# Kernel optimization log

Hardware: AMD Instinct MI355X
Metric: run time of the kernel (lower is better)

## Reference

```python
import jax, jax.numpy as jnp
import numpy as np

D_MODEL = 512
NHEAD = 8
WINDOW = 128
DFF = 2048
LN_EPS = 1e-5


def _layernorm(x, g, b):
    mu = jnp.mean(x, axis=-1, keepdims=True)
    var = jnp.mean(jnp.square(x - mu), axis=-1, keepdims=True)
    return (x - mu) * jax.lax.rsqrt(var + LN_EPS) * g + b


def setup_inputs() -> dict:
    key = jax.random.key(0)
    ks = jax.random.split(key, 8)
    d, dff = D_MODEL, DFF
    s = 0.02
    return {
        "x": jax.random.normal(ks[0], (1, 4096, d), dtype=jnp.float32),
        # weights stored [in, out] (transposed vs torch nn.Linear.weight)
        "qkv_w": jax.random.normal(ks[1], (d, 3 * d), dtype=jnp.float32) * s,
        "qkv_b": jnp.zeros((3 * d,), jnp.float32),
        "out_w": jax.random.normal(ks[2], (d, d), dtype=jnp.float32) * s,
        "out_b": jnp.zeros((d,), jnp.float32),
        "ln1_g": jnp.ones((d,), jnp.float32),
        "ln1_b": jnp.zeros((d,), jnp.float32),
        "w1": jax.random.normal(ks[3], (d, dff), dtype=jnp.float32) * s,
        "b1": jnp.zeros((dff,), jnp.float32),
        "w2": jax.random.normal(ks[4], (dff, d), dtype=jnp.float32) * s,
        "b2": jnp.zeros((d,), jnp.float32),
        "ln2_g": jnp.ones((d,), jnp.float32),
        "ln2_b": jnp.zeros((d,), jnp.float32),
    }


def reference(x, qkv_w, qkv_b, out_w, out_b, ln1_g, ln1_b, w1, b1, w2, b2, ln2_g, ln2_b):
    B, S, d = x.shape
    H = NHEAD
    hd = d // H
    # qkv projection -> [B,S,3,H,hd] -> q,k,v each [B,H,S,hd]
    qkv = (x @ qkv_w + qkv_b).reshape(B, S, 3, H, hd)
    q = jnp.transpose(qkv[:, :, 0], (0, 2, 1, 3))
    k = jnp.transpose(qkv[:, :, 1], (0, 2, 1, 3))
    v = jnp.transpose(qkv[:, :, 2], (0, 2, 1, 3))
    # NOTE: faithful to source, scale is 1/sqrt(d_model), NOT 1/sqrt(head_dim)
    scores = jnp.einsum('bhqd,bhkd->bhqk', q, k) / jnp.sqrt(jnp.float32(d))
    idx = jnp.arange(S)
    band = jnp.abs(idx[:, None] - idx[None, :]) <= WINDOW  # [S,S] window mask
    scores = jnp.where(band[None, None], scores, -jnp.inf)
    attn = jax.nn.softmax(scores, axis=-1)
    o = jnp.einsum('bhqk,bhkd->bhqd', attn, v)
    o = jnp.transpose(o, (0, 2, 1, 3)).reshape(B, S, d)
    attn_out = o @ out_w + out_b
    x1 = _layernorm(x + attn_out, ln1_g, ln1_b)
    ff = jax.nn.relu(x1 @ w1 + b1) @ w2 + b2  # dropout=0 / eval mode
    return _layernorm(x1 + ff, ln2_g, ln2_b)
```

## Files before the change

kernel.cpp:

```cpp
#include <hip/hip_runtime.h>
#include <math.h>

constexpr int D      = 512;
constexpr int NH     = 8;
constexpr int HD     = 64;
constexpr int WIN    = 128;
constexpr int DFF    = 2048;
constexpr int SEQ    = 4096;
constexpr float LN_EPS = 1e-5f;

typedef float f32x4 __attribute__((ext_vector_type(4)));
typedef __bf16 bf16x8 __attribute__((ext_vector_type(8)));

__device__ __forceinline__ unsigned short f2bf(float f) {
    union { float f; unsigned u; } v; v.f = f;
    unsigned r = v.u + 0x7FFF + ((v.u >> 16) & 1);
    return (unsigned short)(r >> 16);
}
__device__ __forceinline__ float bf2f(unsigned short u) {
    union { unsigned u; float f; } v; v.u = (unsigned)u << 16; return v.f;
}

__device__ __forceinline__ void gload16(const void* g, void* l) {
    __builtin_amdgcn_global_load_lds(
        (const __attribute__((address_space(1))) unsigned int*)g,
        (__attribute__((address_space(3))) unsigned int*)l,
        16, 0, 0);
}

__device__ __forceinline__ int xcd_swizzle() {
    const int orig = blockIdx.x + gridDim.x * (blockIdx.y + gridDim.y * blockIdx.z);
    const int nwg  = gridDim.x * gridDim.y * gridDim.z;
    return (orig & 7) * (nwg >> 3) + (orig >> 3);
}

__global__ __launch_bounds__(256) void prep(
    const float* __restrict__ x, unsigned short* __restrict__ xb,
    const float* __restrict__ qkv_w, const float* __restrict__ out_w,
    const float* __restrict__ w1,    const float* __restrict__ w2,
    unsigned short* __restrict__ qkvw_t, unsigned short* __restrict__ outw_t,
    unsigned short* __restrict__ w1_t,   unsigned short* __restrict__ w2_t)
{
    const int b = blockIdx.x;
    if (b < 1024) {
        int i = b * 2048 + threadIdx.x * 8;
        float4 v0 = *(const float4*)(x + i);
        float4 v1 = *(const float4*)(x + i + 4);
        ushort4 u0 = make_ushort4(f2bf(v0.x), f2bf(v0.y), f2bf(v0.z), f2bf(v0.w));
        ushort4 u1 = make_ushort4(f2bf(v1.x), f2bf(v1.y), f2bf(v1.z), f2bf(v1.w));
        *(ushort4*)(xb + i) = u0;
        *(ushort4*)(xb + i + 4) = u1;
        return;
    }
    __shared__ float t[32][33];
    const int b2 = b - 1024;
    const float* W; unsigned short* Wt; int K, N, nt, kt;
    if (b2 < 768)       { W = qkv_w; Wt = qkvw_t; K = 512;  N = 1536; nt = b2 % 48;          kt = b2 / 48; }
    else if (b2 < 1024) { W = out_w; Wt = outw_t; K = 512;  N = 512;  nt = (b2 - 768) % 16;  kt = (b2 - 768) / 16; }
    else if (b2 < 2048) { W = w1;    Wt = w1_t;   K = 512;  N = 2048; nt = (b2 - 1024) % 64; kt = (b2 - 1024) / 64; }
    else                { W = w2;    Wt = w2_t;   K = 2048; N = 512;  nt = (b2 - 2048) % 16; kt = (b2 - 2048) / 16; }
    const int tx = threadIdx.x & 31, ty = threadIdx.x >> 5;
    const int n0 = nt * 32, k0 = kt * 32;
    #pragma unroll
    for (int r = 0; r < 4; ++r)
        t[ty + r * 8][tx] = W[(size_t)(k0 + ty + r * 8) * N + n0 + tx];
    __syncthreads();
    #pragma unroll
    for (int r = 0; r < 4; ++r)
        Wt[(size_t)(n0 + ty + r * 8) * K + k0 + tx] = f2bf(t[tx][ty + r * 8]);
}

__device__ __forceinline__ void stage64_8w(
    const unsigned short* __restrict__ A, const unsigned short* __restrict__ Bt,
    int K, int m0, int n0, int k0, char* buf, int tid)
{
    const int row = tid >> 2;
    const int kb  = (tid & 3) * 16;
    const char* pa = (const char*)A  + ((size_t)(m0 + row) * K + k0) * 2 + kb;
    const char* pb = (const char*)Bt + ((size_t)(n0 + row) * K + k0) * 2 + kb;
    char* dst = buf + tid * 16;
    gload16(pa,      dst);
    gload16(pa + 64, dst + 8192);
    gload16(pb,      dst + 16384);
    gload16(pb + 64, dst + 24576);
}

__device__ __forceinline__ void gemm_core_db8(
    const unsigned short* __restrict__ A, const unsigned short* __restrict__ Bt,
    int K, int m0, int n0, int kbeg, int kend, char* lds, f32x4 acc[4][2])
{
    const int tid  = threadIdx.x;
    const int lane = tid & 63;
    const int wave = tid >> 6;
    const int wr = wave >> 2, wc = wave & 3;
    const int lr = lane & 15, lk = lane >> 4;
    const int aoff = ((wr * 64 + lr) << 6) + (lk << 4);
    const int boff = 16384 + ((wc * 32 + lr) << 6) + (lk << 4);

    stage64_8w(A, Bt, K, m0, n0, kbeg, lds, tid);
    __syncthreads();

    int cur = 0;
    for (int k0 = kbeg; k0 < kend; k0 += 64) {
        char* bufc = lds + cur * 32768;
        if (k0 + 64 < kend)
            stage64_8w(A, Bt, K, m0, n0, k0 + 64, lds + (cur ^ 1) * 32768, tid);

        bf16x8 af[2][4], bfv[2][2];
        #pragma unroll
        for (int m = 0; m < 4; ++m) {
            af[0][m] = *(const bf16x8*)(bufc +        aoff + m * 1024);
            af[1][m] = *(const bf16x8*)(bufc + 8192 + aoff + m * 1024);
        }
        #pragma unroll
        for (int n = 0; n < 2; ++n) {
            bfv[0][n] = *(const bf16x8*)(bufc +        boff + n * 1024);
            bfv[1][n] = *(const bf16x8*)(bufc + 8192 + boff + n * 1024);
        }
        #pragma unroll
        for (int ks = 0; ks < 2; ++ks)
            #pragma unroll
            for (int m = 0; m < 4; ++m)
                #pragma unroll
                for (int n = 0; n < 2; ++n)
                    acc[m][n] = __builtin_amdgcn_mfma_f32_16x16x32_bf16(
                        af[ks][m], bfv[ks][n], acc[m][n], 0, 0, 0);

        __syncthreads();
        cur ^= 1;
    }
}

template <bool RELU, bool OUT_BF16>
__global__ __launch_bounds__(512) void gemm_mfma(
    const unsigned short* __restrict__ A,
    const unsigned short* __restrict__ Bt,
    const float* __restrict__ bias,
    void* __restrict__ Cv, int M, int N, int K)
{
    __shared__ __align__(16) char lds[65536];
    const int lane = threadIdx.x & 63;
    const int wave = threadIdx.x >> 6;
    const int wr = wave >> 2, wc = wave & 3;
    const int lr = lane & 15, lk = lane >> 4;

    const int wg = xcd_swizzle();
    const int bx = wg % gridDim.x, by = wg / gridDim.x;
    const int m0 = by * 128, n0 = bx * 128;

    f32x4 acc[4][2];
    #pragma unroll
    for (int m = 0; m < 4; ++m)
        #pragma unroll
        for (int n = 0; n < 2; ++n) acc[m][n] = f32x4{0.f, 0.f, 0.f, 0.f};

    gemm_core_db8(A, Bt, K, m0, n0, 0, K, lds, acc);

    const int col0 = n0 + wc * 32 + lr;
    const int row0 = m0 + wr * 64 + lk * 4;
    #pragma unroll
    for (int m = 0; m < 4; ++m)
        #pragma unroll
        for (int n = 0; n < 2; ++n) {
            int col = col0 + n * 16;
            float bv = bias[col];
            #pragma unroll
            for (int j = 0; j < 4; ++j) {
                int row = row0 + m * 16 + j;
                float v = acc[m][n][j] + bv;
                if (RELU) v = fmaxf(v, 0.0f);
                if (OUT_BF16)
                    ((unsigned short*)Cv)[(size_t)row * N + col] = f2bf(v);
                else
                    ((float*)Cv)[(size_t)row * N + col] = v;
            }
        }
}

__global__ __launch_bounds__(512) void gemm_splitk(
    const unsigned short* __restrict__ A,
    const unsigned short* __restrict__ Bt,
    const float* __restrict__ bias,
    unsigned short* __restrict__ P, int M, int N, int K, int Kc)
{
    __shared__ __align__(16) char lds[65536];
    const int lane = threadIdx.x & 63;
    const int wave = threadIdx.x >> 6;
    const int wr = wave >> 2, wc = wave & 3;
    const int lr = lane & 15, lk = lane >> 4;

    const int wg = xcd_swizzle();
    const int bx = wg % gridDim.x;
    const int tmp = wg / gridDim.x;
    const int by = tmp % gridDim.y;
    const int zc = tmp / gridDim.y;
    const int m0 = by * 128, n0 = bx * 128;

    f32x4 acc[4][2];
    #pragma unroll
    for (int m = 0; m < 4; ++m)
        #pragma unroll
        for (int n = 0; n < 2; ++n) acc[m][n] = f32x4{0.f, 0.f, 0.f, 0.f};

    gemm_core_db8(A, Bt, K, m0, n0, zc * Kc, zc * Kc + Kc, lds, acc);

    unsigned short* Cp = P + (size_t)zc * M * N;
    const int col0 = n0 + wc * 32 + lr;
    const int row0 = m0 + wr * 64 + lk * 4;
    #pragma unroll
    for (int m = 0; m < 4; ++m)
        #pragma unroll
        for (int n = 0; n < 2; ++n) {
            int col = col0 + n * 16;
            float bv = (zc == 0) ? bias[col] : 0.0f;
            #pragma unroll
            for (int j = 0; j < 4; ++j) {
                int row = row0 + m * 16 + j;
                Cp[(size_t)row * N + col] = f2bf(acc[m][n][j] + bv);
            }
        }
}

__global__ __launch_bounds__(512) void gemm_qkv(
    const unsigned short* __restrict__ A,
    const unsigned short* __restrict__ Bt,
    const float* __restrict__ bias,
    unsigned short* __restrict__ qb,
    unsigned short* __restrict__ kb,
    unsigned short* __restrict__ vtb)
{
    constexpr int N = 3 * D, K = D;
    __shared__ __align__(16) char lds[65536];
    const int lane = threadIdx.x & 63;
    const int wave = threadIdx.x >> 6;
    const int wr = wave >> 2, wc = wave & 3;
    const int lr = lane & 15, lk = lane >> 4;

    const int wg = xcd_swizzle();
    const int bx = wg % gridDim.x, by = wg / gridDim.x;
    const int m0 = by * 128, n0 = bx * 128;

    f32x4 acc[4][2];
    #pragma unroll
    for (int m = 0; m < 4; ++m)
        #pragma unroll
        for (int n = 0; n < 2; ++n) acc[m][n] = f32x4{0.f, 0.f, 0.f, 0.f};

    gemm_core_db8(A, Bt, K, m0, n0, 0, K, lds, acc);

    const int col0 = n0 + wc * 32 + lr;
    const int row0 = m0 + wr * 64 + lk * 4;
    const int region = n0 >> 9;
    #pragma unroll
    for (int m = 0; m < 4; ++m)
        #pragma unroll
        for (int n = 0; n < 2; ++n) {
            const int col = col0 + n * 16;
            const float bv = bias[col];
            const int rowm = row0 + m * 16;
            if (region == 2) {
                const int cc = col - 1024, hh = cc >> 6, dd = cc & 63;
                ushort4 u = make_ushort4(f2bf(acc[m][n][0] + bv),
                                         f2bf(acc[m][n][1] + bv),
                                         f2bf(acc[m][n][2] + bv),
                                         f2bf(acc[m][n][3] + bv));
                *(ushort4*)&vtb[((size_t)(hh * 64 + dd)) * SEQ + rowm] = u;
            } else {
                const int cc = col - region * 512, hh = cc >> 6, dd = cc & 63;
                unsigned short* dst = (region == 0) ? qb : kb;
                #pragma unroll
                for (int j = 0; j < 4; ++j)
                    dst[((size_t)hh * SEQ + rowm + j) * 64 + dd] =
                        f2bf(acc[m][n][j] + bv);
            }
        }
}

__global__ __launch_bounds__(256) void attn_mfma(
    const unsigned short* __restrict__ qb,
    const unsigned short* __restrict__ kb,
    const unsigned short* __restrict__ vtb,
    unsigned short* __restrict__ o)
{
    constexpr float SCALE_L2E = 0.044194173824159216f * 1.4426950408889634f;
    __shared__ __align__(16) unsigned short P_lds[4][16][72];

    const int lane = threadIdx.x & 63;
    const int w    = threadIdx.x >> 6;

    const int wg = xcd_swizzle();
    const int i0 = (wg & 63) * 64;
    const int h  = wg >> 6;
    const int lr = lane & 15, lg = lane >> 4;

    const unsigned short* qh = qb  + (size_t)h * SEQ * 64;
    const unsigned short* kh = kb  + (size_t)h * SEQ * 64;
    const unsigned short* vh = vtb + (size_t)h * 64 * SEQ;

    bf16x8 bq[2];
    {
        const unsigned short* qrow = qh + (size_t)(i0 + w * 16 + lr) * 64 + lg * 8;
        bq[0] = *(const bf16x8*)qrow;
        bq[1] = *(const bf16x8*)(qrow + 32);
    }

    f32x4 accO[4];
    #pragma unroll
    for (int n = 0; n < 4; ++n) accO[n] = f32x4{0.f, 0.f, 0.f, 0.f};
    float lsum = 0.0f;
    const int iq = i0 + w * 16 + lr;

    auto loadKV = [&](int c, bf16x8 (&ak)[2][4], bf16x8 (&bv)[2][4]) {
        const int j0 = i0 - WIN + c * 64;
        #pragma unroll
        for (int m = 0; m < 4; ++m) {
            const unsigned short* kr = kh + (size_t)(j0 + m * 16 + lr) * 64 + lg * 8;
            ak[0][m] = *(const bf16x8*)kr;
            ak[1][m] = *(const bf16x8*)(kr + 32);
        }
        #pragma unroll
        for (int n = 0; n < 4; ++n) {
            const unsigned short* vr = vh + (size_t)(n * 16 + lr) * SEQ + j0 + lg * 8;
            bv[0][n] = *(const bf16x8*)vr;
            bv[1][n] = *(const bf16x8*)(vr + 32);
        }
    };

    auto computeChunk = [&](int c, const bf16x8 (&ak)[2][4], const bf16x8 (&bv)[2][4]) {
        const int j0 = i0 - WIN + c * 64;
        f32x4 accS[4];
        #pragma unroll
        for (int m = 0; m < 4; ++m) {
            accS[m] = f32x4{0.f, 0.f, 0.f, 0.f};
            #pragma unroll
            for (int s = 0; s < 2; ++s)
                accS[m] = __builtin_amdgcn_mfma_f32_16x16x32_bf16(
                    ak[s][m], bq[s], accS[m], 0, 0, 0);
        }
        #pragma unroll
        for (int m = 0; m < 4; ++m) {
            const int kbase = j0 + m * 16 + lg * 4;
            int d0 = kbase + 0 - iq; bool v0 = (d0 >= -WIN) && (d0 <= WIN);
            int d1 = kbase + 1 - iq; bool v1 = (d1 >= -WIN) && (d1 <= WIN);
            int d2 = kbase + 2 - iq; bool v2 = (d2 >= -WIN) && (d2 <= WIN);
            int d3 = kbase + 3 - iq; bool v3 = (d3 >= -WIN) && (d3 <= WIN);
            float p0 = v0 ? exp2f(accS[m][0] * SCALE_L2E) : 0.0f;
            float p1 = v1 ? exp2f(accS[m][1] * SCALE_L2E) : 0.0f;
            float p2 = v2 ? exp2f(accS[m][2] * SCALE_L2E) : 0.0f;
            float p3 = v3 ? exp2f(accS[m][3] * SCALE_L2E) : 0.0f;
            lsum += (p0 + p1) + (p2 + p3);
            ushort4 pk = make_ushort4(f2bf(p0), f2bf(p1), f2bf(p2), f2bf(p3));
            *(ushort4*)&P_lds[w][lr][m * 16 + lg * 4] = pk;
        }
        bf16x8 pa[2];
        pa[0] = *(const bf16x8*)&P_lds[w][lr][lg * 8];
        pa[1] = *(const bf16x8*)&P_lds[w][lr][32 + lg * 8];
        #pragma unroll
        for (int n = 0; n < 4; ++n)
            #pragma unroll
            for (int s = 0; s < 2; ++s)
                accO[n] = __builtin_amdgcn_mfma_f32_16x16x32_bf16(
                    pa[s], bv[s][n], accO[n], 0, 0, 0);
    };

    const int cmin = (i0 >= WIN) ? 0 : ((WIN - i0 + 63) >> 6);
    const int cmaxv = (SEQ + WIN - 64 - i0) >> 6;
    const int cmax = cmaxv < 4 ? cmaxv : 4;

    bf16x8 akA[2][4], bvA[2][4], akB[2][4], bvB[2][4];
    loadKV(cmin, akA, bvA);
    for (int c = cmin; c <= cmax; c += 2) {
        if (c + 1 <= cmax) loadKV(c + 1, akB, bvB);
        computeChunk(c, akA, bvA);
        if (c + 1 > cmax) break;
        if (c + 2 <= cmax) loadKV(c + 2, akA, bvA);
        computeChunk(c + 1, akB, bvB);
    }

    lsum += __shfl_xor(lsum, 16, 64);
    lsum += __shfl_xor(lsum, 32, 64);
    float rinv[4];
    #pragma unroll
    for (int j = 0; j < 4; ++j)
        rinv[j] = 1.0f / __shfl(lsum, lg * 4 + j, 64);

    #pragma unroll
    for (int n = 0; n < 4; ++n)
        #pragma unroll
        for (int j = 0; j < 4; ++j) {
            int row = i0 + w * 16 + lg * 4 + j;
            int col = h * 64 + n * 16 + lr;
            o[(size_t)row * D + col] = f2bf(accO[n][j] * rinv[j]);
        }
}

template <int NP, bool RES_BF16, bool OUT_BF16>
__global__ __launch_bounds__(256) void add_ln(
    const void* __restrict__ res, const unsigned short* __restrict__ P,
    size_t pstride,
    const float* __restrict__ g, const float* __restrict__ beta,
    void* __restrict__ out)
{
    const int wave = threadIdx.x >> 6;
    const int lane = threadIdx.x & 63;
    const int row = blockIdx.x * 4 + wave;
    const size_t rbase = (size_t)row * D;

    float v[2][4];
    float sum = 0.0f, sumsq = 0.0f;
    #pragma unroll
    for (int e = 0; e < 2; ++e) {
        const int c = lane * 4 + e * 256;
        float z0, z1, z2, z3;
        if (RES_BF16) {
            ushort4 u = *(const ushort4*)((const unsigned short*)res + rbase + c);
            z0 = bf2f(u.x); z1 = bf2f(u.y); z2 = bf2f(u.z); z3 = bf2f(u.w);
        } else {
            float4 f = *(const float4*)((const float*)res + rbase + c);
            z0 = f.x; z1 = f.y; z2 = f.z; z3 = f.w;
        }
        #pragma unroll
        for (int p = 0; p < NP; ++p) {
            ushort4 u = *(const ushort4*)(P + p * pstride + rbase + c);
            z0 += bf2f(u.x); z1 += bf2f(u.y); z2 += bf2f(u.z); z3 += bf2f(u.w);
        }
        v[e][0] = z0; v[e][1] = z1; v[e][2] = z2; v[e][3] = z3;
        sum   += (z0 + z1) + (z2 + z3);
        sumsq += (z0 * z0 + z1 * z1) + (z2 * z2 + z3 * z3);
    }
    #pragma unroll
    for (int off = 32; off; off >>= 1) {
        sum   += __shfl_xor(sum, off, 64);
        sumsq += __shfl_xor(sumsq, off, 64);
    }
    const float mu   = sum * (1.0f / D);
    const float var  = sumsq * (1.0f / D) - mu * mu;
    const float rstd = rsqrtf(var + LN_EPS);

    #pragma unroll
    for (int e = 0; e < 2; ++e) {
        const int c = lane * 4 + e * 256;
        float4 gv = *(const float4*)(g + c);
        float4 bb = *(const float4*)(beta + c);
        float r0 = (v[e][0] - mu) * rstd * gv.x + bb.x;
        float r1 = (v[e][1] - mu) * rstd * gv.y + bb.y;
        float r2 = (v[e][2] - mu) * rstd * gv.z + bb.z;
        float r3 = (v[e][3] - mu) * rstd * gv.w + bb.w;
        if (OUT_BF16) {
            ushort4 u = make_ushort4(f2bf(r0), f2bf(r1), f2bf(r2), f2bf(r3));
            *(ushort4*)((unsigned short*)out + rbase + c) = u;
        } else {
            *(float4*)((float*)out + rbase + c) = make_float4(r0, r1, r2, r3);
        }
    }
}

extern "C" void kernel_launch(void* const* d_in, const int* in_sizes, int n_in,
                              void* d_out, int out_size, void* d_ws, size_t ws_size,
                              hipStream_t stream)
{
    const float* x      = (const float*)d_in[0];
    const float* qkv_w  = (const float*)d_in[1];
    const float* qkv_b  = (const float*)d_in[2];
    const float* out_w  = (const float*)d_in[3];
    const float* out_b  = (const float*)d_in[4];
    const float* ln1_g  = (const float*)d_in[5];
    const float* ln1_b  = (const float*)d_in[6];
    const float* w1     = (const float*)d_in[7];
    const float* b1     = (const float*)d_in[8];
    const float* w2     = (const float*)d_in[9];
    const float* b2     = (const float*)d_in[10];
    const float* ln2_g  = (const float*)d_in[11];
    const float* ln2_b  = (const float*)d_in[12];
    float* out = (float*)d_out;

    constexpr size_t MiB = 1u << 20;
    char* base = (char*)d_ws;
    unsigned short* xb     = (unsigned short*)(base + 0);
    unsigned short* qkvw_t = (unsigned short*)(base + 4 * MiB);
    unsigned short* outw_t = (unsigned short*)(base + 5 * MiB + 512 * 1024);
    unsigned short* w1_t   = (unsigned short*)(base + 6 * MiB);
    unsigned short* w2_t   = (unsigned short*)(base + 8 * MiB);
    unsigned short* qbuf   = (unsigned short*)(base + 10 * MiB);
    unsigned short* kbuf   = (unsigned short*)(base + 14 * MiB);
    unsigned short* vtbuf  = (unsigned short*)(base + 18 * MiB);
    unsigned short* o_b    = (unsigned short*)(base + 22 * MiB);
    unsigned short* pOut   = (unsigned short*)(base + 26 * MiB);
    unsigned short* x1b    = (unsigned short*)(base + 34 * MiB);
    unsigned short* ff1b   = (unsigned short*)(base + 38 * MiB);
    unsigned short* pFF2   = (unsigned short*)(base + 54 * MiB);

    prep<<<4096, 256, 0, stream>>>(x, xb, qkv_w, out_w, w1, w2,
                                   qkvw_t, outw_t, w1_t, w2_t);

    gemm_qkv<<<dim3(3 * D / 128, SEQ / 128), 512, 0, stream>>>(
        xb, qkvw_t, qkv_b, qbuf, kbuf, vtbuf);

    attn_mfma<<<dim3(SEQ / 64, NH), 256, 0, stream>>>(qbuf, kbuf, vtbuf, o_b);

    gemm_splitk<<<dim3(D / 128, SEQ / 128, 2), 512, 0, stream>>>(
        o_b, outw_t, out_b, pOut, SEQ, D, D, D / 2);

    add_ln<2, false, true><<<SEQ / 4, 256, 0, stream>>>(
        x, pOut, (size_t)SEQ * D, ln1_g, ln1_b, x1b);

    gemm_mfma<true, true><<<dim3(DFF / 128, SEQ / 128), 512, 0, stream>>>(
        x1b, w1_t, b1, ff1b, SEQ, DFF, D);

    gemm_splitk<<<dim3(D / 128, SEQ / 128, 4), 512, 0, stream>>>(
        ff1b, w2_t, b2, pFF2, SEQ, D, DFF, DFF / 4);

    add_ln<4, true, false><<<SEQ / 4, 256, 0, stream>>>(
        x1b, pFF2, (size_t)SEQ * D, ln2_g, ln2_b, out);
}
```

Baseline: 90.93 us.

## Widen QKV and FF1 GEMM tiles to 128x256 with K-step 32

Adds a new GEMM core with 128x256 output tiles and a K step of 32, double-buffered in 48KB of LDS, and uses it for the QKV and FF1 GEMMs. Each wave now computes a 64x64 sub-tile, which raises MFMA work per LDS fragment load and halves the grid size. The split-K path keeps the old 128x128 core. The attention kernel's software-pipelined K/V prefetch (ping-pong register sets) is replaced by a simple per-chunk loop with bounds skipping. This cuts register pressure, but K/V global loads are no longer overlapped with compute.

```diff
diff --git a/kernel.cpp b/kernel.cpp
--- a/kernel.cpp
+++ b/kernel.cpp
@@ -70,24 +70,23 @@
         Wt[(size_t)(n0 + ty + r * 8) * K + k0 + tx] = f2bf(t[tx][ty + r * 8]);
 }
 
-__device__ __forceinline__ void stage64_8w(
+__device__ __forceinline__ void stage32_256(
     const unsigned short* __restrict__ A, const unsigned short* __restrict__ Bt,
     int K, int m0, int n0, int k0, char* buf, int tid)
 {
     const int row = tid >> 2;
     const int kb  = (tid & 3) * 16;
-    const char* pa = (const char*)A  + ((size_t)(m0 + row) * K + k0) * 2 + kb;
-    const char* pb = (const char*)Bt + ((size_t)(n0 + row) * K + k0) * 2 + kb;
-    char* dst = buf + tid * 16;
-    gload16(pa,      dst);
-    gload16(pa + 64, dst + 8192);
-    gload16(pb,      dst + 16384);
-    gload16(pb + 64, dst + 24576);
-}
-
-__device__ __forceinline__ void gemm_core_db8(
+    gload16((const char*)A  + ((size_t)(m0 + row) * K + k0) * 2 + kb,
+            buf + tid * 16);
+    gload16((const char*)Bt + ((size_t)(n0 + row) * K + k0) * 2 + kb,
+            buf + 8192 + tid * 16);
+    gload16((const char*)Bt + ((size_t)(n0 + 128 + row) * K + k0) * 2 + kb,
+            buf + 16384 + tid * 16);
+}
+
+__device__ __forceinline__ void gemm_core_256(
     const unsigned short* __restrict__ A, const unsigned short* __restrict__ Bt,
-    int K, int m0, int n0, int kbeg, int kend, char* lds, f32x4 acc[4][2])
+    int K, int m0, int n0, char* lds, f32x4 acc[4][4])
 {
     const int tid  = threadIdx.x;
     const int lane = tid & 63;
@@ -95,50 +94,44 @@
     const int wr = wave >> 2, wc = wave & 3;
     const int lr = lane & 15, lk = lane >> 4;
     const int aoff = ((wr * 64 + lr) << 6) + (lk << 4);
-    const int boff = 16384 + ((wc * 32 + lr) << 6) + (lk << 4);
-
-    stage64_8w(A, Bt, K, m0, n0, kbeg, lds, tid);
+    const int boff = 8192 + ((wc * 64 + lr) << 6) + (lk << 4);
+
+    stage32_256(A, Bt, K, m0, n0, 0, lds, tid);
     __syncthreads();
 
     int cur = 0;
-    for (int k0 = kbeg; k0 < kend; k0 += 64) {
-        char* bufc = lds + cur * 32768;
-        if (k0 + 64 < kend)
-            stage64_8w(A, Bt, K, m0, n0, k0 + 64, lds + (cur ^ 1) * 32768, tid);
-
-        bf16x8 af[2][4], bfv[2][2];
-        #pragma unroll
-        for (int m = 0; m < 4; ++m) {
-            af[0][m] = *(const bf16x8*)(bufc +        aoff + m * 1024);
-            af[1][m] = *(const bf16x8*)(bufc + 8192 + aoff + m * 1024);
-        }
-        #pragma unroll
-        for (int n = 0; n < 2; ++n) {
-            bfv[0][n] = *(const bf16x8*)(bufc +        boff + n * 1024);
-            bfv[1][n] = *(const bf16x8*)(bufc + 8192 + boff + n * 1024);
-        }
-        #pragma unroll
-        for (int ks = 0; ks < 2; ++ks)
+    for (int k0 = 0; k0 < K; k0 += 32) {
+        char* bufc = lds + cur * 24576;
+        if (k0 + 32 < K)
+            stage32_256(A, Bt, K, m0, n0, k0 + 32, lds + (cur ^ 1) * 24576, tid);
+
+        bf16x8 af[4], bfv[4];
+        #pragma unroll
+        for (int m = 0; m < 4; ++m)
+            af[m] = *(const bf16x8*)(bufc + aoff + m * 1024);
+        #pragma unroll
+        for (int n = 0; n < 4; ++n)
+            bfv[n] = *(const bf16x8*)(bufc + boff + n * 1024);
+
+        #pragma unroll
+        for (int m = 0; m < 4; ++m)
             #pragma unroll
-            for (int m = 0; m < 4; ++m)
-                #pragma unroll
-                for (int n = 0; n < 2; ++n)
-                    acc[m][n] = __builtin_amdgcn_mfma_f32_16x16x32_bf16(
-                        af[ks][m], bfv[ks][n], acc[m][n], 0, 0, 0);
+            for (int n = 0; n < 4; ++n)
+                acc[m][n] = __builtin_amdgcn_mfma_f32_16x16x32_bf16(
+                    af[m], bfv[n], acc[m][n], 0, 0, 0);
 
         __syncthreads();
         cur ^= 1;
     }
 }
 
-template <bool RELU, bool OUT_BF16>
-__global__ __launch_bounds__(512) void gemm_mfma(
+__global__ __launch_bounds__(512) void gemm_ff1(
     const unsigned short* __restrict__ A,
     const unsigned short* __restrict__ Bt,
     const float* __restrict__ bias,
-    void* __restrict__ Cv, int M, int N, int K)
-{
-    __shared__ __align__(16) char lds[65536];
+    unsigned short* __restrict__ C, int M, int N, int K)
+{
+    __shared__ __align__(16) char lds[49152];
     const int lane = threadIdx.x & 63;
     const int wave = threadIdx.x >> 6;
     const int wr = wave >> 2, wc = wave & 3;
@@ -146,77 +139,29 @@
 
     const int wg = xcd_swizzle();
     const int bx = wg % gridDim.x, by = wg / gridDim.x;
-    const int m0 = by * 128, n0 = bx * 128;
-
-    f32x4 acc[4][2];
+    const int m0 = by * 128, n0 = bx * 256;
+
+    f32x4 acc[4][4];
     #pragma unroll
     for (int m = 0; m < 4; ++m)
         #pragma unroll
-        for (int n = 0; n < 2; ++n) acc[m][n] = f32x4{0.f, 0.f, 0.f, 0.f};
-
-    gemm_core_db8(A, Bt, K, m0, n0, 0, K, lds, acc);
-
-    const int col0 = n0 + wc * 32 + lr;
+        for (int n = 0; n < 4; ++n) acc[m][n] = f32x4{0.f, 0.f, 0.f, 0.f};
+
+    gemm_core_256(A, Bt, K, m0, n0, lds, acc);
+
+    const int col0 = n0 + wc * 64 + lr;
     const int row0 = m0 + wr * 64 + lk * 4;
     #pragma unroll
     for (int m = 0; m < 4; ++m)
         #pragma unroll
-        for (int n = 0; n < 2; ++n) {
+        for (int n = 0; n < 4; ++n) {
             int col = col0 + n * 16;
             float bv = bias[col];
             #pragma unroll
             for (int j = 0; j < 4; ++j) {
                 int row = row0 + m * 16 + j;
-                float v = acc[m][n][j] + bv;
-                if (RELU) v = fmaxf(v, 0.0f);
-                if (OUT_BF16)
-                    ((unsigned short*)Cv)[(size_t)row * N + col] = f2bf(v);
-                else
-                    ((float*)Cv)[(size_t)row * N + col] = v;
-            }
-        }
-}
-
-__global__ __launch_bounds__(512) void gemm_splitk(
-    const unsigned short* __restrict__ A,
-    const unsigned short* __restrict__ Bt,
-    const float* __restrict__ bias,
-    unsigned short* __restrict__ P, int M, int N, int K, int Kc)
-{
-    __shared__ __align__(16) char lds[65536];
-    const int lane = threadIdx.x & 63;
-    const int wave = threadIdx.x >> 6;
-    const int wr = wave >> 2, wc = wave & 3;
-    const int lr = lane & 15, lk = lane >> 4;
-
-    const int wg = xcd_swizzle();
-    const int bx = wg % gridDim.x;
-    const int tmp = wg / gridDim.x;
-    const int by = tmp % gridDim.y;
-    const int zc = tmp / gridDim.y;
-    const int m0 = by * 128, n0 = bx * 128;
-
-    f32x4 acc[4][2];
-    #pragma unroll
-    for (int m = 0; m < 4; ++m)
-        #pragma unroll
-        for (int n = 0; n < 2; ++n) acc[m][n] = f32x4{0.f, 0.f, 0.f, 0.f};
-
-    gemm_core_db8(A, Bt, K, m0, n0, zc * Kc, zc * Kc + Kc, lds, acc);
-
-    unsigned short* Cp = P + (size_t)zc * M * N;
-    const int col0 = n0 + wc * 32 + lr;
-    const int row0 = m0 + wr * 64 + lk * 4;
-    #pragma unroll
-    for (int m = 0; m < 4; ++m)
-        #pragma unroll
-        for (int n = 0; n < 2; ++n) {
-            int col = col0 + n * 16;
-            float bv = (zc == 0) ? bias[col] : 0.0f;
-            #pragma unroll
-            for (int j = 0; j < 4; ++j) {
-                int row = row0 + m * 16 + j;
-                Cp[(size_t)row * N + col] = f2bf(acc[m][n][j] + bv);
+                float v = fmaxf(acc[m][n][j] + bv, 0.0f);
+                C[(size_t)row * N + col] = f2bf(v);
             }
         }
 }
@@ -229,8 +174,8 @@
     unsigned short* __restrict__ kb,
     unsigned short* __restrict__ vtb)
 {
-    constexpr int N = 3 * D, K = D;
-    __shared__ __align__(16) char lds[65536];
+    constexpr int K = D;
+    __shared__ __align__(16) char lds[49152];
     const int lane = threadIdx.x & 63;
     const int wave = threadIdx.x >> 6;
     const int wr = wave >> 2, wc = wave & 3;
@@ -238,23 +183,23 @@
 
     const int wg = xcd_swizzle();
     const int bx = wg % gridDim.x, by = wg / gridDim.x;
-    const int m0 = by * 128, n0 = bx * 128;
-
-    f32x4 acc[4][2];
+    const int m0 = by * 128, n0 = bx * 256;
+
+    f32x4 acc[4][4];
     #pragma unroll
     for (int m = 0; m < 4; ++m)
         #pragma unroll
-        for (int n = 0; n < 2; ++n) acc[m][n] = f32x4{0.f, 0.f, 0.f, 0.f};
-
-    gemm_core_db8(A, Bt, K, m0, n0, 0, K, lds, acc);
-
-    const int col0 = n0 + wc * 32 + lr;
+        for (int n = 0; n < 4; ++n) acc[m][n] = f32x4{0.f, 0.f, 0.f, 0.f};
+
+    gemm_core_256(A, Bt, K, m0, n0, lds, acc);
+
+    const int col0 = n0 + wc * 64 + lr;
     const int row0 = m0 + wr * 64 + lk * 4;
     const int region = n0 >> 9;
     #pragma unroll
     for (int m = 0; m < 4; ++m)
         #pragma unroll
-        for (int n = 0; n < 2; ++n) {
+        for (int n = 0; n < 4; ++n) {
             const int col = col0 + n * 16;
             const float bv = bias[col];
             const int rowm = row0 + m * 16;
@@ -276,6 +221,111 @@
         }
 }
 
+__device__ __forceinline__ void stage64_8w(
+    const unsigned short* __restrict__ A, const unsigned short* __restrict__ Bt,
+    int K, int m0, int n0, int k0, char* buf, int tid)
+{
+    const int row = tid >> 2;
+    const int kb  = (tid & 3) * 16;
+    const char* pa = (const char*)A  + ((size_t)(m0 + row) * K + k0) * 2 + kb;
+    const char* pb = (const char*)Bt + ((size_t)(n0 + row) * K + k0) * 2 + kb;
+    char* dst = buf + tid * 16;
+    gload16(pa,      dst);
+    gload16(pa + 64, dst + 8192);
+    gload16(pb,      dst + 16384);
+    gload16(pb + 64, dst + 24576);
+}
+
+__device__ __forceinline__ void gemm_core_db8(
+    const unsigned short* __restrict__ A, const unsigned short* __restrict__ Bt,
+    int K, int m0, int n0, int kbeg, int kend, char* lds, f32x4 acc[4][2])
+{
+    const int tid  = threadIdx.x;
+    const int lane = tid & 63;
+    const int wave = tid >> 6;
+    const int wr = wave >> 2, wc = wave & 3;
+    const int lr = lane & 15, lk = lane >> 4;
+    const int aoff = ((wr * 64 + lr) << 6) + (lk << 4);
+    const int boff = 16384 + ((wc * 32 + lr) << 6) + (lk << 4);
+
+    stage64_8w(A, Bt, K, m0, n0, kbeg, lds, tid);
+    __syncthreads();
+
+    int cur = 0;
+    for (int k0 = kbeg; k0 < kend; k0 += 64) {
+        char* bufc = lds + cur * 32768;
+        if (k0 + 64 < kend)
+            stage64_8w(A, Bt, K, m0, n0, k0 + 64, lds + (cur ^ 1) * 32768, tid);
+
+        bf16x8 af[2][4], bfv[2][2];
+        #pragma unroll
+        for (int m = 0; m < 4; ++m) {
+            af[0][m] = *(const bf16x8*)(bufc +        aoff + m * 1024);
+            af[1][m] = *(const bf16x8*)(bufc + 8192 + aoff + m * 1024);
+        }
+        #pragma unroll
+        for (int n = 0; n < 2; ++n) {
+            bfv[0][n] = *(const bf16x8*)(bufc +        boff + n * 1024);
+            bfv[1][n] = *(const bf16x8*)(bufc + 8192 + boff + n * 1024);
+        }
+        #pragma unroll
+        for (int ks = 0; ks < 2; ++ks)
+            #pragma unroll
+            for (int m = 0; m < 4; ++m)
+                #pragma unroll
+                for (int n = 0; n < 2; ++n)
+                    acc[m][n] = __builtin_amdgcn_mfma_f32_16x16x32_bf16(
+                        af[ks][m], bfv[ks][n], acc[m][n], 0, 0, 0);
+
+        __syncthreads();
+        cur ^= 1;
+    }
+}
+
+__global__ __launch_bounds__(512) void gemm_splitk(
+    const unsigned short* __restrict__ A,
+    const unsigned short* __restrict__ Bt,
+    const float* __restrict__ bias,
+    unsigned short* __restrict__ P, int M, int N, int K, int Kc)
+{
+    __shared__ __align__(16) char lds[65536];
+    const int lane = threadIdx.x & 63;
+    const int wave = threadIdx.x >> 6;
+    const int wr = wave >> 2, wc = wave & 3;
+    const int lr = lane & 15, lk = lane >> 4;
+
+    const int wg = xcd_swizzle();
+    const int bx = wg % gridDim.x;
+    const int tmp = wg / gridDim.x;
+    const int by = tmp % gridDim.y;
+    const int zc = tmp / gridDim.y;
+    const int m0 = by * 128, n0 = bx * 128;
+
+    f32x4 acc[4][2];
+    #pragma unroll
+    for (int m = 0; m < 4; ++m)
+        #pragma unroll
+        for (int n = 0; n < 2; ++n) acc[m][n] = f32x4{0.f, 0.f, 0.f, 0.f};
+
+    gemm_core_db8(A, Bt, K, m0, n0, zc * Kc, zc * Kc + Kc, lds, acc);
+
+    unsigned short* Cp = P + (size_t)zc * M * N;
+    const int col0 = n0 + wc * 32 + lr;
+    const int row0 = m0 + wr * 64 + lk * 4;
+    #pragma unroll
+    for (int m = 0; m < 4; ++m)
+        #pragma unroll
+        for (int n = 0; n < 2; ++n) {
+            int col = col0 + n * 16;
+            float bv = (zc == 0) ? bias[col] : 0.0f;
+            #pragma unroll
+            for (int j = 0; j < 4; ++j) {
+                int row = row0 + m * 16 + j;
+                Cp[(size_t)row * N + col] = f2bf(acc[m][n][j] + bv);
+            }
+        }
+}
+
 __global__ __launch_bounds__(256) void attn_mfma(
     const unsigned short* __restrict__ qb,
     const unsigned short* __restrict__ kb,
@@ -310,24 +360,25 @@
     float lsum = 0.0f;
     const int iq = i0 + w * 16 + lr;
 
-    auto loadKV = [&](int c, bf16x8 (&ak)[2][4], bf16x8 (&bv)[2][4]) {
+    for (int c = 0; c < 5; ++c) {
         const int j0 = i0 - WIN + c * 64;
+        if (j0 < 0 || j0 >= SEQ) continue;
+
+        bf16x8 ak[2][4];
         #pragma unroll
         for (int m = 0; m < 4; ++m) {
             const unsigned short* kr = kh + (size_t)(j0 + m * 16 + lr) * 64 + lg * 8;
             ak[0][m] = *(const bf16x8*)kr;
             ak[1][m] = *(const bf16x8*)(kr + 32);
         }
+        bf16x8 bv[2][4];
         #pragma unroll
         for (int n = 0; n < 4; ++n) {
             const unsigned short* vr = vh + (size_t)(n * 16 + lr) * SEQ + j0 + lg * 8;
             bv[0][n] = *(const bf16x8*)vr;
             bv[1][n] = *(const bf16x8*)(vr + 32);
         }
-    };
-
-    auto computeChunk = [&](int c, const bf16x8 (&ak)[2][4], const bf16x8 (&bv)[2][4]) {
-        const int j0 = i0 - WIN + c * 64;
+
         f32x4 accS[4];
         #pragma unroll
         for (int m = 0; m < 4; ++m) {
@@ -337,6 +388,7 @@
                 accS[m] = __builtin_amdgcn_mfma_f32_16x16x32_bf16(
                     ak[s][m], bq[s], accS[m], 0, 0, 0);
         }
+
         #pragma unroll
         for (int m = 0; m < 4; ++m) {
             const int kbase = j0 + m * 16 + lg * 4;
@@ -352,29 +404,17 @@
             ushort4 pk = make_ushort4(f2bf(p0), f2bf(p1), f2bf(p2), f2bf(p3));
             *(ushort4*)&P_lds[w][lr][m * 16 + lg * 4] = pk;
         }
+
         bf16x8 pa[2];
         pa[0] = *(const bf16x8*)&P_lds[w][lr][lg * 8];
         pa[1] = *(const bf16x8*)&P_lds[w][lr][32 + lg * 8];
+
         #pragma unroll
         for (int n = 0; n < 4; ++n)
             #pragma unroll
             for (int s = 0; s < 2; ++s)
                 accO[n] = __builtin_amdgcn_mfma_f32_16x16x32_bf16(
                     pa[s], bv[s][n], accO[n], 0, 0, 0);
-    };
-
-    const int cmin = (i0 >= WIN) ? 0 : ((WIN - i0 + 63) >> 6);
-    const int cmaxv = (SEQ + WIN - 64 - i0) >> 6;
-    const int cmax = cmaxv < 4 ? cmaxv : 4;
-
-    bf16x8 akA[2][4], bvA[2][4], akB[2][4], bvB[2][4];
-    loadKV(cmin, akA, bvA);
-    for (int c = cmin; c <= cmax; c += 2) {
-        if (c + 1 <= cmax) loadKV(c + 1, akB, bvB);
-        computeChunk(c, akA, bvA);
-        if (c + 1 > cmax) break;
-        if (c + 2 <= cmax) loadKV(c + 2, akA, bvA);
-        computeChunk(c + 1, akB, bvB);
     }
 
     lsum += __shfl_xor(lsum, 16, 64);
@@ -493,7 +533,7 @@
     prep<<<4096, 256, 0, stream>>>(x, xb, qkv_w, out_w, w1, w2,
                                    qkvw_t, outw_t, w1_t, w2_t);
 
-    gemm_qkv<<<dim3(3 * D / 128, SEQ / 128), 512, 0, stream>>>(
+    gemm_qkv<<<dim3(3 * D / 256, SEQ / 128), 512, 0, stream>>>(
         xb, qkvw_t, qkv_b, qbuf, kbuf, vtbuf);
 
     attn_mfma<<<dim3(SEQ / 64, NH), 256, 0, stream>>>(qbuf, kbuf, vtbuf, o_b);
@@ -504,7 +544,7 @@
     add_ln<2, false, true><<<SEQ / 4, 256, 0, stream>>>(
         x, pOut, (size_t)SEQ * D, ln1_g, ln1_b, x1b);
 
-    gemm_mfma<true, true><<<dim3(DFF / 128, SEQ / 128), 512, 0, stream>>>(
+    gemm_ff1<<<dim3(DFF / 256, SEQ / 128), 512, 0, stream>>>(
         x1b, w1_t, b1, ff1b, SEQ, DFF, D);
 
     gemm_splitk<<<dim3(D / 128, SEQ / 128, 4), 512, 0, stream>>>(
```

Measured after the change: 98.11 us. +7.9%, slower.

## Switch GEMMs to 32x32x16 MFMA with 4-wave blocks and swizzled LDS

Applied to the files above, without the earlier changes.

All GEMM kernels move from 8 waves using 16x16x32 MFMA tiles to 4 waves, each computing a 64x64 sub-tile with 32x32x16 bf16 MFMA. The LDS staging layout gains an XOR swizzle on 16-byte chunks to reduce bank conflicts. Epilogues are adapted to the 32x32 accumulator layout. The attention kernel also drops its double-buffered K/V register prefetch in favor of a simple loop, trading latency hiding for lower register pressure.

```diff
diff --git a/kernel.cpp b/kernel.cpp
--- a/kernel.cpp
+++ b/kernel.cpp
@@ -9,7 +9,8 @@
 constexpr int SEQ    = 4096;
 constexpr float LN_EPS = 1e-5f;
 
-typedef float f32x4 __attribute__((ext_vector_type(4)));
+typedef float f32x4  __attribute__((ext_vector_type(4)));
+typedef float f32x16 __attribute__((ext_vector_type(16)));
 typedef __bf16 bf16x8 __attribute__((ext_vector_type(8)));
 
 __device__ __forceinline__ unsigned short f2bf(float f) {
@@ -70,61 +71,70 @@
         Wt[(size_t)(n0 + ty + r * 8) * K + k0 + tx] = f2bf(t[tx][ty + r * 8]);
 }
 
-__device__ __forceinline__ void stage64_8w(
+__device__ __forceinline__ void stage_v2(
     const unsigned short* __restrict__ A, const unsigned short* __restrict__ Bt,
     int K, int m0, int n0, int k0, char* buf, int tid)
 {
-    const int row = tid >> 2;
-    const int kb  = (tid & 3) * 16;
-    const char* pa = (const char*)A  + ((size_t)(m0 + row) * K + k0) * 2 + kb;
-    const char* pb = (const char*)Bt + ((size_t)(n0 + row) * K + k0) * 2 + kb;
-    char* dst = buf + tid * 16;
-    gload16(pa,      dst);
-    gload16(pa + 64, dst + 8192);
-    gload16(pb,      dst + 16384);
-    gload16(pb + 64, dst + 24576);
-}
-
-__device__ __forceinline__ void gemm_core_db8(
+    const int s1 = (tid & 2) >> 1;
+    #pragma unroll
+    for (int r = 0; r < 2; ++r) {
+        const int row = (tid >> 2) + r * 64;
+        const int sw  = (row >> 1) & 1;
+        const int kb  = s1 * 32 + (((tid & 1) ^ sw) << 4);
+        const char* pa = (const char*)A  + ((size_t)(m0 + row) * K + k0) * 2 + kb;
+        const char* pb = (const char*)Bt + ((size_t)(n0 + row) * K + k0) * 2 + kb;
+        char* dst = buf + r * 4096 + tid * 16;
+        gload16(pa,      dst);
+        gload16(pa + 64, dst + 8192);
+        gload16(pb,      dst + 16384);
+        gload16(pb + 64, dst + 24576);
+    }
+}
+
+__device__ __forceinline__ void gemm_core_v2(
     const unsigned short* __restrict__ A, const unsigned short* __restrict__ Bt,
-    int K, int m0, int n0, int kbeg, int kend, char* lds, f32x4 acc[4][2])
-{
-    const int tid  = threadIdx.x;
-    const int lane = tid & 63;
-    const int wave = tid >> 6;
-    const int wr = wave >> 2, wc = wave & 3;
-    const int lr = lane & 15, lk = lane >> 4;
-    const int aoff = ((wr * 64 + lr) << 6) + (lk << 4);
-    const int boff = 16384 + ((wc * 32 + lr) << 6) + (lk << 4);
-
-    stage64_8w(A, Bt, K, m0, n0, kbeg, lds, tid);
+    int K, int m0, int n0, int kbeg, int kend, char* lds, f32x16 acc[2][2])
+{
+    const int tid   = threadIdx.x;
+    const int lane  = tid & 63;
+    const int wave  = tid >> 6;
+    const int wr = wave >> 1, wc = wave & 1;
+    const int l31 = lane & 31;
+    const int kg  = lane >> 5;
+    const int sw  = (lane >> 1) & 1;
+    const int kgx = (kg ^ sw) << 4;
+
+    const int abase = ((wr * 64 + l31) << 6) + kgx;
+    const int bbase = 16384 + ((wc * 64 + l31) << 6) + kgx;
+
+    stage_v2(A, Bt, K, m0, n0, kbeg, lds, tid);
     __syncthreads();
 
     int cur = 0;
     for (int k0 = kbeg; k0 < kend; k0 += 64) {
         char* bufc = lds + cur * 32768;
         if (k0 + 64 < kend)
-            stage64_8w(A, Bt, K, m0, n0, k0 + 64, lds + (cur ^ 1) * 32768, tid);
-
-        bf16x8 af[2][4], bfv[2][2];
-        #pragma unroll
-        for (int m = 0; m < 4; ++m) {
-            af[0][m] = *(const bf16x8*)(bufc +        aoff + m * 1024);
-            af[1][m] = *(const bf16x8*)(bufc + 8192 + aoff + m * 1024);
-        }
-        #pragma unroll
-        for (int n = 0; n < 2; ++n) {
-            bfv[0][n] = *(const bf16x8*)(bufc +        boff + n * 1024);
-            bfv[1][n] = *(const bf16x8*)(bufc + 8192 + boff + n * 1024);
-        }
-        #pragma unroll
-        for (int ks = 0; ks < 2; ++ks)
-            #pragma unroll
-            for (int m = 0; m < 4; ++m)
+            stage_v2(A, Bt, K, m0, n0, k0 + 64, lds + (cur ^ 1) * 32768, tid);
+
+        bf16x8 af[4][2], bf[4][2];
+        #pragma unroll
+        for (int ks = 0; ks < 4; ++ks) {
+            const int off = (ks >> 1) * 8192 + (ks & 1) * 32;
+            #pragma unroll
+            for (int mf = 0; mf < 2; ++mf)
+                af[ks][mf] = *(const bf16x8*)(bufc + abase + off + mf * 2048);
+            #pragma unroll
+            for (int nf = 0; nf < 2; ++nf)
+                bf[ks][nf] = *(const bf16x8*)(bufc + bbase + off + nf * 2048);
+        }
+        #pragma unroll
+        for (int ks = 0; ks < 4; ++ks)
+            #pragma unroll
+            for (int mf = 0; mf < 2; ++mf)
                 #pragma unroll
-                for (int n = 0; n < 2; ++n)
-                    acc[m][n] = __builtin_amdgcn_mfma_f32_16x16x32_bf16(
-                        af[ks][m], bfv[ks][n], acc[m][n], 0, 0, 0);
+                for (int nf = 0; nf < 2; ++nf)
+                    acc[mf][nf] = __builtin_amdgcn_mfma_f32_32x32x16_bf16(
+                        af[ks][mf], bf[ks][nf], acc[mf][nf], 0, 0, 0);
 
         __syncthreads();
         cur ^= 1;
@@ -132,7 +142,7 @@
 }
 
 template <bool RELU, bool OUT_BF16>
-__global__ __launch_bounds__(512) void gemm_mfma(
+__global__ __launch_bounds__(256) void gemm_mfma(
     const unsigned short* __restrict__ A,
     const unsigned short* __restrict__ Bt,
     const float* __restrict__ bias,
@@ -141,33 +151,34 @@
     __shared__ __align__(16) char lds[65536];
     const int lane = threadIdx.x & 63;
     const int wave = threadIdx.x >> 6;
-    const int wr = wave >> 2, wc = wave & 3;
-    const int lr = lane & 15, lk = lane >> 4;
+    const int wr = wave >> 1, wc = wave & 1;
+    const int l31 = lane & 31, kg = lane >> 5;
 
     const int wg = xcd_swizzle();
     const int bx = wg % gridDim.x, by = wg / gridDim.x;
     const int m0 = by * 128, n0 = bx * 128;
 
-    f32x4 acc[4][2];
-    #pragma unroll
-    for (int m = 0; m < 4; ++m)
-        #pragma unroll
-        for (int n = 0; n < 2; ++n) acc[m][n] = f32x4{0.f, 0.f, 0.f, 0.f};
-
-    gemm_core_db8(A, Bt, K, m0, n0, 0, K, lds, acc);
-
-    const int col0 = n0 + wc * 32 + lr;
-    const int row0 = m0 + wr * 64 + lk * 4;
-    #pragma unroll
-    for (int m = 0; m < 4; ++m)
-        #pragma unroll
-        for (int n = 0; n < 2; ++n) {
-            int col = col0 + n * 16;
-            float bv = bias[col];
-            #pragma unroll
-            for (int j = 0; j < 4; ++j) {
-                int row = row0 + m * 16 + j;
-                float v = acc[m][n][j] + bv;
+    f32x16 acc[2][2];
+    #pragma unroll
+    for (int mf = 0; mf < 2; ++mf)
+        #pragma unroll
+        for (int nf = 0; nf < 2; ++nf)
+            #pragma unroll
+            for (int e = 0; e < 16; ++e) acc[mf][nf][e] = 0.f;
+
+    gemm_core_v2(A, Bt, K, m0, n0, 0, K, lds, acc);
+
+    #pragma unroll
+    for (int mf = 0; mf < 2; ++mf)
+        #pragma unroll
+        for (int nf = 0; nf < 2; ++nf) {
+            const int col = n0 + wc * 64 + nf * 32 + l31;
+            const float bv = bias[col];
+            const int rowb = m0 + wr * 64 + mf * 32 + 4 * kg;
+            #pragma unroll
+            for (int reg = 0; reg < 16; ++reg) {
+                int row = rowb + (reg & 3) + 8 * (reg >> 2);
+                float v = acc[mf][nf][reg] + bv;
                 if (RELU) v = fmaxf(v, 0.0f);
                 if (OUT_BF16)
                     ((unsigned short*)Cv)[(size_t)row * N + col] = f2bf(v);
@@ -177,7 +188,7 @@
         }
 }
 
-__global__ __launch_bounds__(512) void gemm_splitk(
+__global__ __launch_bounds__(256) void gemm_splitk(
     const unsigned short* __restrict__ A,
     const unsigned short* __restrict__ Bt,
     const float* __restrict__ bias,
@@ -186,8 +197,8 @@
     __shared__ __align__(16) char lds[65536];
     const int lane = threadIdx.x & 63;
     const int wave = threadIdx.x >> 6;
-    const int wr = wave >> 2, wc = wave & 3;
-    const int lr = lane & 15, lk = lane >> 4;
+    const int wr = wave >> 1, wc = wave & 1;
+    const int l31 = lane & 31, kg = lane >> 5;
 
     const int wg = xcd_swizzle();
     const int bx = wg % gridDim.x;
@@ -196,32 +207,33 @@
     const int zc = tmp / gridDim.y;
     const int m0 = by * 128, n0 = bx * 128;
 
-    f32x4 acc[4][2];
-    #pragma unroll
-    for (int m = 0; m < 4; ++m)
-        #pragma unroll
-        for (int n = 0; n < 2; ++n) acc[m][n] = f32x4{0.f, 0.f, 0.f, 0.f};
-
-    gemm_core_db8(A, Bt, K, m0, n0, zc * Kc, zc * Kc + Kc, lds, acc);
+    f32x16 acc[2][2];
+    #pragma unroll
+    for (int mf = 0; mf < 2; ++mf)
+        #pragma unroll
+        for (int nf = 0; nf < 2; ++nf)
+            #pragma unroll
+            for (int e = 0; e < 16; ++e) acc[mf][nf][e] = 0.f;
+
+    gemm_core_v2(A, Bt, K, m0, n0, zc * Kc, zc * Kc + Kc, lds, acc);
 
     unsigned short* Cp = P + (size_t)zc * M * N;
-    const int col0 = n0 + wc * 32 + lr;
-    const int row0 = m0 + wr * 64 + lk * 4;
-    #pragma unroll
-    for (int m = 0; m < 4; ++m)
-        #pragma unroll
-        for (int n = 0; n < 2; ++n) {
-            int col = col0 + n * 16;
-            float bv = (zc == 0) ? bias[col] : 0.0f;
-            #pragma unroll
-            for (int j = 0; j < 4; ++j) {
-                int row = row0 + m * 16 + j;
-                Cp[(size_t)row * N + col] = f2bf(acc[m][n][j] + bv);
+    #pragma unroll
+    for (int mf = 0; mf < 2; ++mf)
+        #pragma unroll
+        for (int nf = 0; nf < 2; ++nf) {
+            const int col = n0 + wc * 64 + nf * 32 + l31;
+            const float bv = (zc == 0) ? bias[col] : 0.0f;
+            const int rowb = m0 + wr * 64 + mf * 32 + 4 * kg;
+            #pragma unroll
+            for (int reg = 0; reg < 16; ++reg) {
+                int row = rowb + (reg & 3) + 8 * (reg >> 2);
+                Cp[(size_t)row * N + col] = f2bf(acc[mf][nf][reg] + bv);
             }
         }
 }
 
-__global__ __launch_bounds__(512) void gemm_qkv(
+__global__ __launch_bounds__(256) void gemm_qkv(
     const unsigned short* __restrict__ A,
     const unsigned short* __restrict__ Bt,
     const float* __restrict__ bias,
@@ -229,49 +241,55 @@
     unsigned short* __restrict__ kb,
     unsigned short* __restrict__ vtb)
 {
-    constexpr int N = 3 * D, K = D;
+    constexpr int K = D;
     __shared__ __align__(16) char lds[65536];
     const int lane = threadIdx.x & 63;
     const int wave = threadIdx.x >> 6;
-    const int wr = wave >> 2, wc = wave & 3;
-    const int lr = lane & 15, lk = lane >> 4;
+    const int wr = wave >> 1, wc = wave & 1;
+    const int l31 = lane & 31, kg = lane >> 5;
 
     const int wg = xcd_swizzle();
     const int bx = wg % gridDim.x, by = wg / gridDim.x;
     const int m0 = by * 128, n0 = bx * 128;
 
-    f32x4 acc[4][2];
-    #pragma unroll
-    for (int m = 0; m < 4; ++m)
-        #pragma unroll
-        for (int n = 0; n < 2; ++n) acc[m][n] = f32x4{0.f, 0.f, 0.f, 0.f};
-
-    gemm_core_db8(A, Bt, K, m0, n0, 0, K, lds, acc);
-
-    const int col0 = n0 + wc * 32 + lr;
-    const int row0 = m0 + wr * 64 + lk * 4;
+    f32x16 acc[2][2];
+    #pragma unroll
+    for (int mf = 0; mf < 2; ++mf)
+        #pragma unroll
+        for (int nf = 0; nf < 2; ++nf)
+            #pragma unroll
+            for (int e = 0; e < 16; ++e) acc[mf][nf][e] = 0.f;
+
+    gemm_core_v2(A, Bt, K, m0, n0, 0, K, lds, acc);
+
     const int region = n0 >> 9;
     #pragma unroll
-    for (int m = 0; m < 4; ++m)
-        #pragma unroll
-        for (int n = 0; n < 2; ++n) {
-            const int col = col0 + n * 16;
+    for (int mf = 0; mf < 2; ++mf)
+        #pragma unroll
+        for (int nf = 0; nf < 2; ++nf) {
+            const int col = n0 + wc * 64 + nf * 32 + l31;
             const float bv = bias[col];
-            const int rowm = row0 + m * 16;
+            const int rowb = m0 + wr * 64 + mf * 32 + 4 * kg;
             if (region == 2) {
                 const int cc = col - 1024, hh = cc >> 6, dd = cc & 63;
-                ushort4 u = make_ushort4(f2bf(acc[m][n][0] + bv),
-                                         f2bf(acc[m][n][1] + bv),
-                                         f2bf(acc[m][n][2] + bv),
-                                         f2bf(acc[m][n][3] + bv));
-                *(ushort4*)&vtb[((size_t)(hh * 64 + dd)) * SEQ + rowm] = u;
+                unsigned short* vbase = vtb + ((size_t)(hh * 64 + dd)) * SEQ;
+                #pragma unroll
+                for (int rq = 0; rq < 4; ++rq) {
+                    ushort4 u = make_ushort4(f2bf(acc[mf][nf][rq * 4 + 0] + bv),
+                                             f2bf(acc[mf][nf][rq * 4 + 1] + bv),
+                                             f2bf(acc[mf][nf][rq * 4 + 2] + bv),
+                                             f2bf(acc[mf][nf][rq * 4 + 3] + bv));
+                    *(ushort4*)&vbase[rowb + 8 * rq] = u;
+                }
             } else {
                 const int cc = col - region * 512, hh = cc >> 6, dd = cc & 63;
                 unsigned short* dst = (region == 0) ? qb : kb;
                 #pragma unroll
-                for (int j = 0; j < 4; ++j)
-                    dst[((size_t)hh * SEQ + rowm + j) * 64 + dd] =
-                        f2bf(acc[m][n][j] + bv);
+                for (int reg = 0; reg < 16; ++reg) {
+                    int row = rowb + (reg & 3) + 8 * (reg >> 2);
+                    dst[((size_t)hh * SEQ + row) * 64 + dd] =
+                        f2bf(acc[mf][nf][reg] + bv);
+                }
             }
         }
 }
@@ -310,24 +328,25 @@
     float lsum = 0.0f;
     const int iq = i0 + w * 16 + lr;
 
-    auto loadKV = [&](int c, bf16x8 (&ak)[2][4], bf16x8 (&bv)[2][4]) {
+    for (int c = 0; c < 5; ++c) {
         const int j0 = i0 - WIN + c * 64;
+        if (j0 < 0 || j0 >= SEQ) continue;
+
+        bf16x8 ak[2][4];
         #pragma unroll
         for (int m = 0; m < 4; ++m) {
             const unsigned short* kr = kh + (size_t)(j0 + m * 16 + lr) * 64 + lg * 8;
             ak[0][m] = *(const bf16x8*)kr;
             ak[1][m] = *(const bf16x8*)(kr + 32);
         }
+        bf16x8 bv[2][4];
         #pragma unroll
         for (int n = 0; n < 4; ++n) {
             const unsigned short* vr = vh + (size_t)(n * 16 + lr) * SEQ + j0 + lg * 8;
             bv[0][n] = *(const bf16x8*)vr;
             bv[1][n] = *(const bf16x8*)(vr + 32);
         }
-    };
-
-    auto computeChunk = [&](int c, const bf16x8 (&ak)[2][4], const bf16x8 (&bv)[2][4]) {
-        const int j0 = i0 - WIN + c * 64;
+
         f32x4 accS[4];
         #pragma unroll
         for (int m = 0; m < 4; ++m) {
@@ -337,6 +356,7 @@
                 accS[m] = __builtin_amdgcn_mfma_f32_16x16x32_bf16(
                     ak[s][m], bq[s], accS[m], 0, 0, 0);
         }
+
         #pragma unroll
         for (int m = 0; m < 4; ++m) {
             const int kbase = j0 + m * 16 + lg * 4;
@@ -352,29 +372,17 @@
             ushort4 pk = make_ushort4(f2bf(p0), f2bf(p1), f2bf(p2), f2bf(p3));
             *(ushort4*)&P_lds[w][lr][m * 16 + lg * 4] = pk;
         }
+
         bf16x8 pa[2];
         pa[0] = *(const bf16x8*)&P_lds[w][lr][lg * 8];
         pa[1] = *(const bf16x8*)&P_lds[w][lr][32 + lg * 8];
+
         #pragma unroll
         for (int n = 0; n < 4; ++n)
             #pragma unroll
             for (int s = 0; s < 2; ++s)
                 accO[n] = __builtin_amdgcn_mfma_f32_16x16x32_bf16(
                     pa[s], bv[s][n], accO[n], 0, 0, 0);
-    };
-
-    const int cmin = (i0 >= WIN) ? 0 : ((WIN - i0 + 63) >> 6);
-    const int cmaxv = (SEQ + WIN - 64 - i0) >> 6;
-    const int cmax = cmaxv < 4 ? cmaxv : 4;
-
-    bf16x8 akA[2][4], bvA[2][4], akB[2][4], bvB[2][4];
-    loadKV(cmin, akA, bvA);
-    for (int c = cmin; c <= cmax; c += 2) {
-        if (c + 1 <= cmax) loadKV(c + 1, akB, bvB);
-        computeChunk(c, akA, bvA);
-        if (c + 1 > cmax) break;
-        if (c + 2 <= cmax) loadKV(c + 2, akA, bvA);
-        computeChunk(c + 1, akB, bvB);
     }
 
     lsum += __shfl_xor(lsum, 16, 64);
@@ -493,21 +501,21 @@
     prep<<<4096, 256, 0, stream>>>(x, xb, qkv_w, out_w, w1, w2,
                                    qkvw_t, outw_t, w1_t, w2_t);
 
-    gemm_qkv<<<dim3(3 * D / 128, SEQ / 128), 512, 0, stream>>>(
+    gemm_qkv<<<dim3(3 * D / 128, SEQ / 128), 256, 0, stream>>>(
         xb, qkvw_t, qkv_b, qbuf, kbuf, vtbuf);
 
     attn_mfma<<<dim3(SEQ / 64, NH), 256, 0, stream>>>(qbuf, kbuf, vtbuf, o_b);
 
-    gemm_splitk<<<dim3(D / 128, SEQ / 128, 2), 512, 0, stream>>>(
+    gemm_splitk<<<dim3(D / 128, SEQ / 128, 2), 256, 0, stream>>>(
         o_b, outw_t, out_b, pOut, SEQ, D, D, D / 2);
 
     add_ln<2, false, true><<<SEQ / 4, 256, 0, stream>>>(
         x, pOut, (size_t)SEQ * D, ln1_g, ln1_b, x1b);
 
-    gemm_mfma<true, true><<<dim3(DFF / 128, SEQ / 128), 512, 0, stream>>>(
+    gemm_mfma<true, true><<<dim3(DFF / 128, SEQ / 128), 256, 0, stream>>>(
         x1b, w1_t, b1, ff1b, SEQ, DFF, D);
 
-    gemm_splitk<<<dim3(D / 128, SEQ / 128, 4), 512, 0, stream>>>(
+    gemm_splitk<<<dim3(D / 128, SEQ / 128, 4), 256, 0, stream>>>(
         ff1b, w2_t, b2, pFF2, SEQ, D, DFF, DFF / 4);
 
     add_ln<4, true, false><<<SEQ / 4, 256, 0, stream>>>(
```

Result: slower. 96.83 us (+6.5%).
